# Kernel tuning notes

Measured on AMD Instinct MI355X. Metric: run time of the kernel, lower is better.

Reference implementation:

```python
import jax, jax.numpy as jnp
import numpy as np

ALPHA = 1.0  # initial_alpha; forward uses self.alpha which stays at init value

def setup_inputs() -> dict:
    key = jax.random.key(0)
    k1, k2, k3, k4 = jax.random.split(key, 4)
    B, T, N, C, K = 8, 32, 2048, 64, 32
    R_seq = jax.random.normal(k1, (B, T, N, C), dtype=jnp.float32)
    W = jax.random.normal(k2, (K, C), dtype=jnp.float32) * (1.0 / np.sqrt(C))
    b = jax.random.normal(k3, (K,), dtype=jnp.float32) * 0.01
    cent = jax.random.normal(k4, (K, C), dtype=jnp.float32)
    centroids = cent / jnp.linalg.norm(cent, axis=1, keepdims=True)  # xavier + L2-normalize rows
    return {"R_seq": R_seq, "W": W, "b": b, "centroids": centroids}

def reference(R_seq, W, b, centroids):
    B, T, N, C = R_seq.shape
    K = centroids.shape[0]
    r = R_seq.reshape(B * T, N, C)                       # (BT, N, C)
    logits = (jnp.einsum('mnc,kc->mnk', r, W) + b) * ALPHA
    a = jax.nn.softmax(logits, axis=-1)                  # (BT, N, K)
    # NetVLAD algebraic decomposition: v_k = a_k^T r - (sum_n a_nk) * c_k
    v = jnp.einsum('mnk,mnc->mkc', a, r) - a.sum(axis=1)[:, :, None] * centroids[None]
    return v.reshape(B, T, K, C)
```

## Files before the change

kernel.cpp:

```cpp
#include <hip/hip_runtime.h>
#include <stdint.h>

typedef __attribute__((ext_vector_type(8))) short bf16x8;
typedef __attribute__((ext_vector_type(4))) short bf16x4;
typedef __attribute__((ext_vector_type(4))) float f32x4;

#define WAVES 4
#define RT_STRIDE 36
#define RT_LDS_SHORTS (64 * RT_STRIDE)
#define A_STRIDE 40
#define A_LDS_SHORTS (32 * A_STRIDE)
#define WAVE_LDS (RT_LDS_SHORTS + A_LDS_SHORTS)
#define W_LDS_OFF (WAVES * WAVE_LDS)
#define SMEM_SHORTS (W_LDS_OFF + 2048)
#define VB_STRIDE 68
#define NITER 2
#define WS_STRIDE 2080

static __device__ __forceinline__ bf16x8 cvt8(float4 a, float4 b) {
    union { int i[4]; bf16x8 v; } u;
    asm("v_cvt_pk_bf16_f32 %0, %1, %2" : "=v"(u.i[0]) : "v"(a.x), "v"(a.y));
    asm("v_cvt_pk_bf16_f32 %0, %1, %2" : "=v"(u.i[1]) : "v"(a.z), "v"(a.w));
    asm("v_cvt_pk_bf16_f32 %0, %1, %2" : "=v"(u.i[2]) : "v"(b.x), "v"(b.y));
    asm("v_cvt_pk_bf16_f32 %0, %1, %2" : "=v"(u.i[3]) : "v"(b.z), "v"(b.w));
    return u.v;
}

static __device__ __forceinline__ float row_sum16(float x) {
    union fi { float f; int i; };
    fi a, b; a.f = x;
    b.i = __builtin_amdgcn_mov_dpp(a.i, 0x128, 0xf, 0xf, false); a.f += b.f;
    b.i = __builtin_amdgcn_mov_dpp(a.i, 0x124, 0xf, 0xf, false); a.f += b.f;
    b.i = __builtin_amdgcn_mov_dpp(a.i, 0x122, 0xf, 0xf, false); a.f += b.f;
    b.i = __builtin_amdgcn_mov_dpp(a.i, 0x121, 0xf, 0xf, false); a.f += b.f;
    return a.f;
}

__global__ __launch_bounds__(256, 2)
void netvlad_partial(const float* __restrict__ R,
                     const float* __restrict__ W,
                     const float* __restrict__ bias,
                     float* __restrict__ ws)
{
    __shared__ short smem[SMEM_SHORTS];

    const int tid  = threadIdx.x;
    const int wave = tid >> 6;
    const int lane = tid & 63;
    const int l15  = lane & 15;
    const int quad = lane >> 4;
    const int bid  = blockIdx.x;
    const int m    = bid >> 3;
    const int h    = bid & 7;

    short* rt_lds = smem + wave * WAVE_LDS;
    short* a_lds  = rt_lds + RT_LDS_SHORTS;
    short* w_lds  = smem + W_LDS_OFF;

    const float* Rm = R + ((size_t)m * 2048 + (size_t)h * 256) * 64;

#pragma unroll
    for (int kt = 0; kt < 2; ++kt)
#pragma unroll
        for (int cc = 0; cc < 2; ++cc) {
            const int k = kt*16 + l15;
            const int c = cc*32 + quad*8;
            const float* wp = W + k*64 + c;
            bf16x8 wv = cvt8(*(const float4*)wp, *(const float4*)(wp + 4));
            *(bf16x8*)(w_lds + k*64 + (c ^ ((k & 7) << 3))) = wv;
        }

    float bval[2];
    bval[0] = bias[l15];
    bval[1] = bias[16 + l15];

    f32x4 acc[2][4];
#pragma unroll
    for (int kt = 0; kt < 2; ++kt)
#pragma unroll
        for (int ct = 0; ct < 4; ++ct)
            acc[kt][ct] = (f32x4){0.f, 0.f, 0.f, 0.f};
    float suma[2] = {0.f, 0.f};

#pragma unroll 1
    for (int it = 0; it < NITER; ++it) {
        const int n0 = it * (WAVES * 32) + wave * 32;

#pragma unroll
        for (int s = 0; s < 2; ++s) {
            const int n = s*16 + l15;
            bf16x8 af0, af1;
            {
                const float* rp = Rm + (size_t)(n0 + n)*64 + quad*8;
                af0 = cvt8(*(const float4*)rp, *(const float4*)(rp + 4));
            }
            {
                const float* rp = Rm + (size_t)(n0 + n)*64 + 32 + quad*8;
                af1 = cvt8(*(const float4*)rp, *(const float4*)(rp + 4));
            }

#pragma unroll
            for (int e = 0; e < 8; ++e) {
                rt_lds[(quad*8 + e)*RT_STRIDE + n]      = af0[e];
                rt_lds[(32 + quad*8 + e)*RT_STRIDE + n] = af1[e];
            }

            f32x4 d1s[2];
#pragma unroll
            for (int kt = 0; kt < 2; ++kt) {
                const int k = kt*16 + l15;
                const bf16x8 w0 = *(const bf16x8*)(w_lds + k*64 + ((quad*8)      ^ ((k & 7) << 3)));
                const bf16x8 w1 = *(const bf16x8*)(w_lds + k*64 + ((32 + quad*8) ^ ((k & 7) << 3)));
                f32x4 d = (f32x4){0.f, 0.f, 0.f, 0.f};
                d = __builtin_amdgcn_mfma_f32_16x16x32_bf16(af0, w0, d, 0, 0, 0);
                d = __builtin_amdgcn_mfma_f32_16x16x32_bf16(af1, w1, d, 0, 0, 0);
                d1s[kt] = d;
            }

            float a0v[4], a1v[4];
            float a0s = 0.f, a1s = 0.f;
#pragma unroll
            for (int r = 0; r < 4; ++r) {
                float l0 = d1s[0][r] + bval[0];
                float l1 = d1s[1][r] + bval[1];
                float e0 = __expf(l0);
                float e1 = __expf(l1);
                float ss = row_sum16(e0 + e1);
                float rs = __builtin_amdgcn_rcpf(ss);
                a0v[r] = e0 * rs; a1v[r] = e1 * rs;
                a0s += a0v[r]; a1s += a1v[r];
            }
            suma[0] += a0s; suma[1] += a1s;
            union { int i[2]; bf16x4 v; } p0, p1;
            asm("v_cvt_pk_bf16_f32 %0, %1, %2" : "=v"(p0.i[0]) : "v"(a0v[0]), "v"(a0v[1]));
            asm("v_cvt_pk_bf16_f32 %0, %1, %2" : "=v"(p0.i[1]) : "v"(a0v[2]), "v"(a0v[3]));
            asm("v_cvt_pk_bf16_f32 %0, %1, %2" : "=v"(p1.i[0]) : "v"(a1v[0]), "v"(a1v[1]));
            asm("v_cvt_pk_bf16_f32 %0, %1, %2" : "=v"(p1.i[1]) : "v"(a1v[2]), "v"(a1v[3]));
            *(bf16x4*)(a_lds + l15*A_STRIDE        + s*16 + quad*4) = p0.v;
            *(bf16x4*)(a_lds + (16 + l15)*A_STRIDE + s*16 + quad*4) = p1.v;
        }

        bf16x8 a2[2];
#pragma unroll
        for (int kt = 0; kt < 2; ++kt)
            a2[kt] = *(bf16x8*)(a_lds + (kt*16 + l15)*A_STRIDE + quad*8);

#pragma unroll
        for (int ct = 0; ct < 4; ++ct) {
            const short* bp = rt_lds + (ct*16 + l15)*RT_STRIDE + quad*8;
            union { bf16x4 h[2]; bf16x8 v; } b2;
            b2.h[0] = *(const bf16x4*)bp;
            b2.h[1] = *(const bf16x4*)(bp + 4);
#pragma unroll
            for (int kt = 0; kt < 2; ++kt)
                acc[kt][ct] = __builtin_amdgcn_mfma_f32_16x16x32_bf16(a2[kt], b2.v, acc[kt][ct], 0, 0, 0);
        }
    }

#pragma unroll
    for (int kt = 0; kt < 2; ++kt) {
        suma[kt] += __shfl_xor(suma[kt], 16);
        suma[kt] += __shfl_xor(suma[kt], 32);
    }

    float* vbuf = (float*)smem;
    float* suma_buf = (float*)(smem + W_LDS_OFF);
    __syncthreads();
#pragma unroll
    for (int step = 2; step >= 1; step >>= 1) {
        if (wave >= step && wave < 2*step) {
            float* dst = vbuf + (wave - step) * (32 * VB_STRIDE);
#pragma unroll
            for (int kt = 0; kt < 2; ++kt)
#pragma unroll
                for (int ct = 0; ct < 4; ++ct)
#pragma unroll
                    for (int r = 0; r < 4; ++r)
                        dst[(kt*16 + quad*4 + r)*VB_STRIDE + ct*16 + l15] = acc[kt][ct][r];
            if (lane < 16) {
                suma_buf[(wave - step)*32 + lane]      = suma[0];
                suma_buf[(wave - step)*32 + lane + 16] = suma[1];
            }
        }
        __syncthreads();
        if (wave < step) {
            const float* src = vbuf + wave * (32 * VB_STRIDE);
#pragma unroll
            for (int kt = 0; kt < 2; ++kt)
#pragma unroll
                for (int ct = 0; ct < 4; ++ct)
#pragma unroll
                    for (int r = 0; r < 4; ++r)
                        acc[kt][ct][r] += src[(kt*16 + quad*4 + r)*VB_STRIDE + ct*16 + l15];
            suma[0] += suma_buf[wave*32 + l15];
            suma[1] += suma_buf[wave*32 + l15 + 16];
        }
        __syncthreads();
    }

    if (wave == 0) {
        float* wp = ws + (size_t)bid * WS_STRIDE;
#pragma unroll
        for (int kt = 0; kt < 2; ++kt)
#pragma unroll
            for (int r = 0; r < 4; ++r) {
                const int k = kt*16 + quad*4 + r;
#pragma unroll
                for (int ct = 0; ct < 4; ++ct)
                    wp[k*64 + ct*16 + l15] = acc[kt][ct][r];
            }
        if (lane < 16) {
            wp[2048 + lane]      = suma[0];
            wp[2048 + 16 + lane] = suma[1];
        }
    }
}

__global__ __launch_bounds__(512)
void netvlad_combine(const float* __restrict__ ws,
                     const float* __restrict__ cent,
                     float* __restrict__ out)
{
    const int m   = blockIdx.x;
    const int tid = threadIdx.x;
    const float* pb = ws + (size_t)(8*m) * WS_STRIDE;

    const int k  = tid >> 4;
    const int c0 = (tid & 15) << 2;
    const int off = k*64 + c0;

    float s = 0.f;
    float4 v = {0.f, 0.f, 0.f, 0.f};
#pragma unroll
    for (int i = 0; i < 8; ++i) {
        const float* p = pb + (size_t)i * WS_STRIDE;
        s += p[2048 + k];
        const float4 vi = *(const float4*)(p + off);
        v.x += vi.x; v.y += vi.y; v.z += vi.z; v.w += vi.w;
    }

    const float4 cv = *(const float4*)(cent + off);
    float4 o;
    o.x = v.x - s * cv.x;
    o.y = v.y - s * cv.y;
    o.z = v.z - s * cv.z;
    o.w = v.w - s * cv.w;
    *(float4*)(out + (size_t)m * 2048 + off) = o;
}

extern "C" void kernel_launch(void* const* d_in, const int* in_sizes, int n_in,
                              void* d_out, int out_size, void* d_ws, size_t ws_size,
                              hipStream_t stream) {
    (void)in_sizes; (void)n_in; (void)out_size; (void)ws_size;
    const float* R = (const float*)d_in[0];
    const float* W = (const float*)d_in[1];
    const float* b = (const float*)d_in[2];
    const float* c = (const float*)d_in[3];
    float* out = (float*)d_out;
    float* ws  = (float*)d_ws;

    hipLaunchKernelGGL(netvlad_partial, dim3(2048), dim3(256), 0, stream, R, W, b, ws);
    hipLaunchKernelGGL(netvlad_combine, dim3(256), dim3(512), 0, stream, ws, c, out);
}
```

Before: 206.2 us.

## Coalesce R global loads and stage row-major bf16 tile in swizzled LDS

Each lane now loads four 16-byte chunks spaced 16 floats apart within a row, so a group of four lanes covers a full 256-byte row and global reads become more contiguous. The converted bf16 data is written both to a new swizzled row-major LDS buffer, which feeds the logits MFMA operands, and to the transposed buffer used by the aggregation MFMA. Scheduling barriers are added around the phases. In exchange, each wave uses more LDS and does an extra LDS write and read per tile, which may lower occupancy and adds LDS traffic.

```diff
diff --git a/kernel.cpp b/kernel.cpp
--- a/kernel.cpp
+++ b/kernel.cpp
@@ -6,16 +6,18 @@
 typedef __attribute__((ext_vector_type(4))) float f32x4;
 
 #define WAVES 4
-#define RT_STRIDE 36
-#define RT_LDS_SHORTS (64 * RT_STRIDE)
+#define NC_SHORTS (16 * 64)
+#define CN_STRIDE 36
+#define CN_SHORTS (64 * CN_STRIDE)
 #define A_STRIDE 40
-#define A_LDS_SHORTS (32 * A_STRIDE)
-#define WAVE_LDS (RT_LDS_SHORTS + A_LDS_SHORTS)
+#define A_SHORTS (32 * A_STRIDE)
+#define WAVE_LDS (NC_SHORTS + CN_SHORTS + A_SHORTS)
 #define W_LDS_OFF (WAVES * WAVE_LDS)
 #define SMEM_SHORTS (W_LDS_OFF + 2048)
 #define VB_STRIDE 68
 #define NITER 2
 #define WS_STRIDE 2080
+
 
 static __device__ __forceinline__ bf16x8 cvt8(float4 a, float4 b) {
     union { int i[4]; bf16x8 v; } u;
@@ -53,8 +55,9 @@
     const int m    = bid >> 3;
     const int h    = bid & 7;
 
-    short* rt_lds = smem + wave * WAVE_LDS;
-    short* a_lds  = rt_lds + RT_LDS_SHORTS;
+    short* nc_lds = smem + wave * WAVE_LDS;
+    short* cn_lds = nc_lds + NC_SHORTS;
+    short* a_lds  = cn_lds + CN_SHORTS;
     short* w_lds  = smem + W_LDS_OFF;
 
     const float* Rm = R + ((size_t)m * 2048 + (size_t)h * 256) * 64;
@@ -82,28 +85,53 @@
             acc[kt][ct] = (f32x4){0.f, 0.f, 0.f, 0.f};
     float suma[2] = {0.f, 0.f};
 
+    const int r16 = lane >> 2;
+    const int k4  = lane & 3;
+
 #pragma unroll 1
     for (int it = 0; it < NITER; ++it) {
         const int n0 = it * (WAVES * 32) + wave * 32;
 
 #pragma unroll
         for (int s = 0; s < 2; ++s) {
-            const int n = s*16 + l15;
-            bf16x8 af0, af1;
+            const float* lp = Rm + (size_t)(n0 + s*16 + r16)*64 + k4*4;
+            const float4 x0 = *(const float4*)(lp);
+            const float4 x1 = *(const float4*)(lp + 16);
+            const float4 x2 = *(const float4*)(lp + 32);
+            const float4 x3 = *(const float4*)(lp + 48);
+
+            union { int i[8]; short hh[16]; } cv;
+            asm("v_cvt_pk_bf16_f32 %0, %1, %2" : "=v"(cv.i[0]) : "v"(x0.x), "v"(x0.y));
+            asm("v_cvt_pk_bf16_f32 %0, %1, %2" : "=v"(cv.i[1]) : "v"(x0.z), "v"(x0.w));
+            asm("v_cvt_pk_bf16_f32 %0, %1, %2" : "=v"(cv.i[2]) : "v"(x1.x), "v"(x1.y));
+            asm("v_cvt_pk_bf16_f32 %0, %1, %2" : "=v"(cv.i[3]) : "v"(x1.z), "v"(x1.w));
+            asm("v_cvt_pk_bf16_f32 %0, %1, %2" : "=v"(cv.i[4]) : "v"(x2.x), "v"(x2.y));
+            asm("v_cvt_pk_bf16_f32 %0, %1, %2" : "=v"(cv.i[5]) : "v"(x2.z), "v"(x2.w));
+            asm("v_cvt_pk_bf16_f32 %0, %1, %2" : "=v"(cv.i[6]) : "v"(x3.x), "v"(x3.y));
+            asm("v_cvt_pk_bf16_f32 %0, %1, %2" : "=v"(cv.i[7]) : "v"(x3.z), "v"(x3.w));
+
             {
-                const float* rp = Rm + (size_t)(n0 + n)*64 + quad*8;
-                af0 = cvt8(*(const float4*)rp, *(const float4*)(rp + 4));
+                short* ncw = nc_lds + r16*64;
+                const int swr = (r16 & 7) << 3;
+                *(bf16x4*)(ncw + ((k4*4 +  0) ^ swr)) = *(bf16x4*)&cv.hh[0];
+                *(bf16x4*)(ncw + ((k4*4 + 16) ^ swr)) = *(bf16x4*)&cv.hh[4];
+                *(bf16x4*)(ncw + ((k4*4 + 32) ^ swr)) = *(bf16x4*)&cv.hh[8];
+                *(bf16x4*)(ncw + ((k4*4 + 48) ^ swr)) = *(bf16x4*)&cv.hh[12];
             }
             {
-                const float* rp = Rm + (size_t)(n0 + n)*64 + 32 + quad*8;
-                af1 = cvt8(*(const float4*)rp, *(const float4*)(rp + 4));
-            }
-
-#pragma unroll
-            for (int e = 0; e < 8; ++e) {
-                rt_lds[(quad*8 + e)*RT_STRIDE + n]      = af0[e];
-                rt_lds[(32 + quad*8 + e)*RT_STRIDE + n] = af1[e];
-            }
+                const int n = s*16 + r16;
+#pragma unroll
+                for (int j = 0; j < 4; ++j)
+#pragma unroll
+                    for (int e = 0; e < 4; ++e)
+                        cn_lds[(k4*4 + 16*j + e)*CN_STRIDE + n] = cv.hh[4*j + e];
+            }
+
+            __builtin_amdgcn_sched_barrier(0);
+
+            const int swl = (l15 & 7) << 3;
+            const bf16x8 af0 = *(const bf16x8*)(nc_lds + l15*64 + ((quad*8)      ^ swl));
+            const bf16x8 af1 = *(const bf16x8*)(nc_lds + l15*64 + ((32 + quad*8) ^ swl));
 
             f32x4 d1s[2];
 #pragma unroll
@@ -140,6 +168,8 @@
             *(bf16x4*)(a_lds + (16 + l15)*A_STRIDE + s*16 + quad*4) = p1.v;
         }
 
+        __builtin_amdgcn_sched_barrier(0);
+
         bf16x8 a2[2];
 #pragma unroll
         for (int kt = 0; kt < 2; ++kt)
@@ -147,14 +177,16 @@
 
 #pragma unroll
         for (int ct = 0; ct < 4; ++ct) {
-            const short* bp = rt_lds + (ct*16 + l15)*RT_STRIDE + quad*8;
-            union { bf16x4 h[2]; bf16x8 v; } b2;
-            b2.h[0] = *(const bf16x4*)bp;
-            b2.h[1] = *(const bf16x4*)(bp + 4);
+            const short* bp = cn_lds + (ct*16 + l15)*CN_STRIDE + quad*8;
+            union { bf16x4 h2[2]; bf16x8 v; } b2;
+            b2.h2[0] = *(const bf16x4*)bp;
+            b2.h2[1] = *(const bf16x4*)(bp + 4);
 #pragma unroll
             for (int kt = 0; kt < 2; ++kt)
                 acc[kt][ct] = __builtin_amdgcn_mfma_f32_16x16x32_bf16(a2[kt], b2.v, acc[kt][ct], 0, 0, 0);
         }
+
+        __builtin_amdgcn_sched_barrier(0);
     }
 
 #pragma unroll
```

New measurement: 202.9 us. About the same (-1.6%).

## Stream R tiles via async global_load_lds double buffering with manual waitcnt pipeline

Applied to the files above, without the earlier changes.

Replaces the direct per-lane global loads of R with async global_load_lds into per-wave LDS staging buffers. The next sub-tile is issued while the current one is converted and processed, with explicit vmcnt waits and sched barriers. The aim is to hide global memory latency behind the softmax and MFMA work. In exchange it adds LDS use per wave, which may cut occupancy, and relies on manual wait counts being correct.

```diff
diff --git a/kernel.cpp b/kernel.cpp
--- a/kernel.cpp
+++ b/kernel.cpp
@@ -6,16 +6,24 @@
 typedef __attribute__((ext_vector_type(4))) float f32x4;
 
 #define WAVES 4
-#define RT_STRIDE 36
-#define RT_LDS_SHORTS (64 * RT_STRIDE)
+#define RF_FLOATS 1024
+#define RF_SHORTS (2 * RF_FLOATS * 2)
+#define CN_STRIDE 36
+#define CN_SHORTS (64 * CN_STRIDE)
 #define A_STRIDE 40
-#define A_LDS_SHORTS (32 * A_STRIDE)
-#define WAVE_LDS (RT_LDS_SHORTS + A_LDS_SHORTS)
+#define A_SHORTS (32 * A_STRIDE)
+#define WAVE_LDS (RF_SHORTS + CN_SHORTS + A_SHORTS)
 #define W_LDS_OFF (WAVES * WAVE_LDS)
 #define SMEM_SHORTS (W_LDS_OFF + 2048)
 #define VB_STRIDE 68
-#define NITER 2
 #define WS_STRIDE 2080
+
+
+static __device__ __forceinline__ void gload16(const float* g, float* l) {
+    __builtin_amdgcn_global_load_lds(
+        (const __attribute__((address_space(1))) void*)g,
+        (__attribute__((address_space(3))) void*)l, 16, 0, 0);
+}
 
 static __device__ __forceinline__ bf16x8 cvt8(float4 a, float4 b) {
     union { int i[4]; bf16x8 v; } u;
@@ -36,6 +44,83 @@
     return a.f;
 }
 
+#define WAITV(N) do { \
+    asm volatile("s_waitcnt vmcnt(" #N ")" ::: "memory"); \
+    __builtin_amdgcn_sched_barrier(0); } while(0)
+
+#define ISSUE(it_, s_) do { \
+    const float* g_ = gbase + (size_t)(((it_)*128 + (s_)*16) * 64); \
+    float* l_ = rf + (s_)*RF_FLOATS; \
+    gload16(g_,      l_      ); \
+    gload16(g_ + 16, l_ + 256); \
+    gload16(g_ + 32, l_ + 512); \
+    gload16(g_ + 48, l_ + 768); \
+} while(0)
+
+#define PHASE(s_, ...) do { \
+    const float* lb_ = rf + (s_)*RF_FLOATS; \
+    const float* ap_ = lb_ + (quad>>1)*256 + l15*16 + (quad&1)*8; \
+    const float4 f0_ = *(const float4*)(ap_); \
+    const float4 f1_ = *(const float4*)(ap_ + 4); \
+    const float4 f2_ = *(const float4*)(ap_ + 512); \
+    const float4 f3_ = *(const float4*)(ap_ + 516); \
+    const bf16x8 af0_ = cvt8(f0_, f1_); \
+    const bf16x8 af1_ = cvt8(f2_, f3_); \
+    { const int n_ = (s_)*16 + l15; \
+      _Pragma("unroll") \
+      for (int e = 0; e < 8; ++e) { \
+          cn_lds[(quad*8 + e)*CN_STRIDE + n_]      = af0_[e]; \
+          cn_lds[(32 + quad*8 + e)*CN_STRIDE + n_] = af1_[e]; } } \
+    __builtin_amdgcn_sched_barrier(0); \
+    __VA_ARGS__; \
+    f32x4 d1s_[2]; \
+    _Pragma("unroll") \
+    for (int kt = 0; kt < 2; ++kt) { \
+        const int k_ = kt*16 + l15; \
+        const bf16x8 w0_ = *(const bf16x8*)(w_lds + k_*64 + ((quad*8)      ^ ((k_ & 7) << 3))); \
+        const bf16x8 w1_ = *(const bf16x8*)(w_lds + k_*64 + ((32 + quad*8) ^ ((k_ & 7) << 3))); \
+        f32x4 d_ = (f32x4){0.f, 0.f, 0.f, 0.f}; \
+        d_ = __builtin_amdgcn_mfma_f32_16x16x32_bf16(af0_, w0_, d_, 0, 0, 0); \
+        d_ = __builtin_amdgcn_mfma_f32_16x16x32_bf16(af1_, w1_, d_, 0, 0, 0); \
+        d1s_[kt] = d_; } \
+    float a0v_[4], a1v_[4]; float a0s_ = 0.f, a1s_ = 0.f; \
+    _Pragma("unroll") \
+    for (int r = 0; r < 4; ++r) { \
+        float l0_ = d1s_[0][r] + bval[0]; \
+        float l1_ = d1s_[1][r] + bval[1]; \
+        float e0_ = __expf(l0_), e1_ = __expf(l1_); \
+        float ss_ = row_sum16(e0_ + e1_); \
+        float rs_ = __builtin_amdgcn_rcpf(ss_); \
+        a0v_[r] = e0_ * rs_; a1v_[r] = e1_ * rs_; \
+        a0s_ += a0v_[r]; a1s_ += a1v_[r]; } \
+    suma[0] += a0s_; suma[1] += a1s_; \
+    union { int i[2]; bf16x4 v; } p0_, p1_; \
+    asm("v_cvt_pk_bf16_f32 %0, %1, %2" : "=v"(p0_.i[0]) : "v"(a0v_[0]), "v"(a0v_[1])); \
+    asm("v_cvt_pk_bf16_f32 %0, %1, %2" : "=v"(p0_.i[1]) : "v"(a0v_[2]), "v"(a0v_[3])); \
+    asm("v_cvt_pk_bf16_f32 %0, %1, %2" : "=v"(p1_.i[0]) : "v"(a1v_[0]), "v"(a1v_[1])); \
+    asm("v_cvt_pk_bf16_f32 %0, %1, %2" : "=v"(p1_.i[1]) : "v"(a1v_[2]), "v"(a1v_[3])); \
+    *(bf16x4*)(a_lds + l15*A_STRIDE        + (s_)*16 + quad*4) = p0_.v; \
+    *(bf16x4*)(a_lds + (16 + l15)*A_STRIDE + (s_)*16 + quad*4) = p1_.v; \
+} while(0)
+
+#define GEMM2 do { \
+    __builtin_amdgcn_sched_barrier(0); \
+    bf16x8 a2_[2]; \
+    _Pragma("unroll") \
+    for (int kt = 0; kt < 2; ++kt) \
+        a2_[kt] = *(bf16x8*)(a_lds + (kt*16 + l15)*A_STRIDE + quad*8); \
+    _Pragma("unroll") \
+    for (int ct = 0; ct < 4; ++ct) { \
+        const short* bp_ = cn_lds + (ct*16 + l15)*CN_STRIDE + quad*8; \
+        union { bf16x4 h2[2]; bf16x8 v; } b2_; \
+        b2_.h2[0] = *(const bf16x4*)bp_; \
+        b2_.h2[1] = *(const bf16x4*)(bp_ + 4); \
+        _Pragma("unroll") \
+        for (int k2 = 0; k2 < 2; ++k2) \
+            acc[k2][ct] = __builtin_amdgcn_mfma_f32_16x16x32_bf16(a2_[k2], b2_.v, acc[k2][ct], 0, 0, 0); } \
+    __builtin_amdgcn_sched_barrier(0); \
+} while(0)
+
 __global__ __launch_bounds__(256, 2)
 void netvlad_partial(const float* __restrict__ R,
                      const float* __restrict__ W,
@@ -53,8 +138,10 @@
     const int m    = bid >> 3;
     const int h    = bid & 7;
 
-    short* rt_lds = smem + wave * WAVE_LDS;
-    short* a_lds  = rt_lds + RT_LDS_SHORTS;
+    short* wbase  = smem + wave * WAVE_LDS;
+    float* rf     = (float*)wbase;
+    short* cn_lds = wbase + RF_SHORTS;
+    short* a_lds  = wbase + RF_SHORTS + CN_SHORTS;
     short* w_lds  = smem + W_LDS_OFF;
 
     const float* Rm = R + ((size_t)m * 2048 + (size_t)h * 256) * 64;
@@ -82,80 +169,20 @@
             acc[kt][ct] = (f32x4){0.f, 0.f, 0.f, 0.f};
     float suma[2] = {0.f, 0.f};
 
-#pragma unroll 1
-    for (int it = 0; it < NITER; ++it) {
-        const int n0 = it * (WAVES * 32) + wave * 32;
-
-#pragma unroll
-        for (int s = 0; s < 2; ++s) {
-            const int n = s*16 + l15;
-            bf16x8 af0, af1;
-            {
-                const float* rp = Rm + (size_t)(n0 + n)*64 + quad*8;
-                af0 = cvt8(*(const float4*)rp, *(const float4*)(rp + 4));
-            }
-            {
-                const float* rp = Rm + (size_t)(n0 + n)*64 + 32 + quad*8;
-                af1 = cvt8(*(const float4*)rp, *(const float4*)(rp + 4));
-            }
-
-#pragma unroll
-            for (int e = 0; e < 8; ++e) {
-                rt_lds[(quad*8 + e)*RT_STRIDE + n]      = af0[e];
-                rt_lds[(32 + quad*8 + e)*RT_STRIDE + n] = af1[e];
-            }
-
-            f32x4 d1s[2];
-#pragma unroll
-            for (int kt = 0; kt < 2; ++kt) {
-                const int k = kt*16 + l15;
-                const bf16x8 w0 = *(const bf16x8*)(w_lds + k*64 + ((quad*8)      ^ ((k & 7) << 3)));
-                const bf16x8 w1 = *(const bf16x8*)(w_lds + k*64 + ((32 + quad*8) ^ ((k & 7) << 3)));
-                f32x4 d = (f32x4){0.f, 0.f, 0.f, 0.f};
-                d = __builtin_amdgcn_mfma_f32_16x16x32_bf16(af0, w0, d, 0, 0, 0);
-                d = __builtin_amdgcn_mfma_f32_16x16x32_bf16(af1, w1, d, 0, 0, 0);
-                d1s[kt] = d;
-            }
-
-            float a0v[4], a1v[4];
-            float a0s = 0.f, a1s = 0.f;
-#pragma unroll
-            for (int r = 0; r < 4; ++r) {
-                float l0 = d1s[0][r] + bval[0];
-                float l1 = d1s[1][r] + bval[1];
-                float e0 = __expf(l0);
-                float e1 = __expf(l1);
-                float ss = row_sum16(e0 + e1);
-                float rs = __builtin_amdgcn_rcpf(ss);
-                a0v[r] = e0 * rs; a1v[r] = e1 * rs;
-                a0s += a0v[r]; a1s += a1v[r];
-            }
-            suma[0] += a0s; suma[1] += a1s;
-            union { int i[2]; bf16x4 v; } p0, p1;
-            asm("v_cvt_pk_bf16_f32 %0, %1, %2" : "=v"(p0.i[0]) : "v"(a0v[0]), "v"(a0v[1]));
-            asm("v_cvt_pk_bf16_f32 %0, %1, %2" : "=v"(p0.i[1]) : "v"(a0v[2]), "v"(a0v[3]));
-            asm("v_cvt_pk_bf16_f32 %0, %1, %2" : "=v"(p1.i[0]) : "v"(a1v[0]), "v"(a1v[1]));
-            asm("v_cvt_pk_bf16_f32 %0, %1, %2" : "=v"(p1.i[1]) : "v"(a1v[2]), "v"(a1v[3]));
-            *(bf16x4*)(a_lds + l15*A_STRIDE        + s*16 + quad*4) = p0.v;
-            *(bf16x4*)(a_lds + (16 + l15)*A_STRIDE + s*16 + quad*4) = p1.v;
-        }
-
-        bf16x8 a2[2];
-#pragma unroll
-        for (int kt = 0; kt < 2; ++kt)
-            a2[kt] = *(bf16x8*)(a_lds + (kt*16 + l15)*A_STRIDE + quad*8);
-
-#pragma unroll
-        for (int ct = 0; ct < 4; ++ct) {
-            const short* bp = rt_lds + (ct*16 + l15)*RT_STRIDE + quad*8;
-            union { bf16x4 h[2]; bf16x8 v; } b2;
-            b2.h[0] = *(const bf16x4*)bp;
-            b2.h[1] = *(const bf16x4*)(bp + 4);
-#pragma unroll
-            for (int kt = 0; kt < 2; ++kt)
-                acc[kt][ct] = __builtin_amdgcn_mfma_f32_16x16x32_bf16(a2[kt], b2.v, acc[kt][ct], 0, 0, 0);
-        }
-    }
+    const float* gbase = Rm + (size_t)(wave*32 + (lane >> 2))*64 + (lane & 3)*4;
+
+    asm volatile("s_waitcnt vmcnt(0)" ::: "memory");
+    __builtin_amdgcn_sched_barrier(0);
+
+    ISSUE(0, 0);
+    ISSUE(0, 1);
+
+    WAITV(4);  PHASE(0, ISSUE(1, 0));
+    WAITV(4);  PHASE(1, ISSUE(1, 1));
+    GEMM2;
+    WAITV(4);  PHASE(0, (void)0);
+    WAITV(0);  PHASE(1, (void)0);
+    GEMM2;
 
 #pragma unroll
     for (int kt = 0; kt < 2; ++kt) {
```

Measured after the change: 203.4 us. Within noise of the previous version (-1.4%).
